# Kernel tuning notes

Hardware: AMD Instinct MI355X
Metric: run time of the kernel (lower is better)

The kernel has to match this reference:

```python
import jax, jax.numpy as jnp
import numpy as np

ROTARY_DIM = 64
ROPE_THETA = 10000.0
BLOCK_SIZE = 24


def setup_inputs() -> dict:
    key = jax.random.key(0)
    ks = jax.random.split(key, 6)
    B, T_code = 2, 2048
    d_cond, d_code, d_spk, d_model, vocab = 512, 512, 192, 1024, 6561
    cond = jax.random.normal(ks[0], (B, 1, d_cond), dtype=jnp.float32)
    spk = jax.random.normal(ks[1], (B, 1, d_spk), dtype=jnp.float32)
    code = jax.random.randint(ks[2], (B, T_code), 0, vocab, dtype=jnp.int64)
    embed_table = jax.random.normal(ks[3], (vocab, d_code), dtype=jnp.float32)
    W = jax.random.normal(ks[4], (d_cond + d_code + d_spk, d_model), dtype=jnp.float32) * 0.02
    b = jax.random.normal(ks[5], (d_model,), dtype=jnp.float32) * 0.02
    return {"cond": cond, "spk": spk, "code": code,
            "embed_table": embed_table, "W": W, "b": b}


def _rope(T):
    # DitRotary.forward
    pos = jnp.arange(T, dtype=jnp.float32).reshape(-1, 1)          # [T,1]
    theta = 1.0 / ROPE_THETA ** (jnp.arange(0, ROTARY_DIM, 2, dtype=jnp.float32) / ROTARY_DIM)
    idx = pos * theta                                              # [T,32]
    r = jnp.stack([jnp.cos(idx), jnp.sin(idx)])                    # [2,T,32]
    r = jnp.stack((r, r), axis=-1).reshape(2, T, ROTARY_DIM)       # [2,T,64]
    return r[:, None, :, None, :]                                  # [2,1,T,1,64]


def reference(cond, spk, code, embed_table, W, b):
    B, T_code = code.shape
    T = T_code * 2  # max_duration
    d_cond = cond.shape[-1]
    d_code = embed_table.shape[-1]
    code_embed = jnp.repeat(embed_table[code], 2, axis=1)          # [B,T,d_code]
    # concat([cond.repeat, code_embed, spk.repeat]) @ W + b, computed as split
    # matmuls with broadcast (same math, avoids materializing repeats)
    W_cond = W[:d_cond]
    W_code = W[d_cond:d_cond + d_code]
    W_spk = W[d_cond + d_code:]
    code_embeds = (jnp.einsum('btc,cd->btd', code_embed, W_code)
                   + cond @ W_cond + spk @ W_spk + b)              # [B,T,d_model]
    rope = _rope(T)
    # block-causal mask precompute
    blk = jnp.arange(T) // BLOCK_SIZE
    mask = (blk[None, :] - blk[:, None]).reshape(1, 1, T, T)       # int
    return code_embeds, rope, mask
```

## Files before the change

kernel.cpp:

```cpp
#include <hip/hip_runtime.h>
#include <hip/hip_bf16.h>
#include <cstdint>

typedef short short8 __attribute__((ext_vector_type(8)));
typedef float f32x4 __attribute__((ext_vector_type(4)));

#define OUT0_SZ  (2*4096*1024)
#define OUT1_OFF OUT0_SZ
#define OUT2_OFF (OUT0_SZ + 2*4096*64)

__device__ __forceinline__ unsigned short f2bf(float f) {
    unsigned u = __float_as_uint(f);
    unsigned r = (u + 0x7FFFu + ((u >> 16) & 1u)) >> 16;
    return (unsigned short)r;
}

__global__ __launch_bounds__(256) void prep_kernel(
    const float* __restrict__ embed, const int* __restrict__ code,
    const float* __restrict__ cond, const float* __restrict__ spk,
    const float* __restrict__ W, const float* __restrict__ bvec,
    unsigned short* __restrict__ Ag, unsigned short* __restrict__ Wt,
    float* __restrict__ bias)
{
    __shared__ float tile[32][33];
    __shared__ float red[8][32];
    const int bid = blockIdx.x;

    if (bid < 1024) {
        int gtid = bid * 256 + threadIdx.x;
        int r = gtid >> 6;
        int c = (gtid & 63) * 8;
        int cv = code[r];
        const float* s = embed + (size_t)cv * 512 + c;
        float4 f0 = *(const float4*)s;
        float4 f1 = *(const float4*)(s + 4);
        short8 v;
        v[0] = (short)f2bf(f0.x); v[1] = (short)f2bf(f0.y);
        v[2] = (short)f2bf(f0.z); v[3] = (short)f2bf(f0.w);
        v[4] = (short)f2bf(f1.x); v[5] = (short)f2bf(f1.y);
        v[6] = (short)f2bf(f1.z); v[7] = (short)f2bf(f1.w);
        *(short8*)&Ag[(size_t)r * 512 + c] = v;
    } else if (bid < 1536) {
        int idx = bid - 1024;
        int k0 = (idx & 15) * 32;
        int n0 = (idx >> 4) * 32;
        int lx = threadIdx.x & 31;
        int ly = threadIdx.x >> 5;
        #pragma unroll
        for (int rr = 0; rr < 32; rr += 8)
            tile[ly + rr][lx] = W[(size_t)(512 + k0 + ly + rr) * 1024 + n0 + lx];
        __syncthreads();
        #pragma unroll
        for (int rr = 0; rr < 32; rr += 8)
            Wt[(size_t)(n0 + ly + rr) * 512 + k0 + lx] = f2bf(tile[lx][ly + rr]);
    } else {
        int idx = bid - 1536;
        const int b  = idx >> 5;
        const int d0 = (idx & 31) * 32;
        const int dl = threadIdx.x & 31;
        const int ks = threadIdx.x >> 5;
        const int d  = d0 + dl;
        const float* condb = cond + b * 512;
        const float* spkb  = spk + b * 192;
        float acc = 0.f;
        #pragma unroll 8
        for (int i = 0; i < 64; ++i) {
            int k = ks * 64 + i;
            acc = fmaf(condb[k], W[(size_t)k * 1024 + d], acc);
        }
        #pragma unroll 8
        for (int i = 0; i < 24; ++i) {
            int s = ks * 24 + i;
            acc = fmaf(spkb[s], W[(size_t)(1024 + s) * 1024 + d], acc);
        }
        red[ks][dl] = acc;
        __syncthreads();
        if (ks == 0) {
            float t = acc + bvec[d];
            #pragma unroll
            for (int j = 1; j < 8; ++j) t += red[j][dl];
            bias[b * 1024 + d] = t;
        }
    }
}

__global__ __launch_bounds__(256) void main_kernel(
    const unsigned short* __restrict__ Ag, const unsigned short* __restrict__ Wt,
    const float* __restrict__ bias, float* __restrict__ out0,
    float* __restrict__ out1, float* __restrict__ out2)
{
    __shared__ short8 AsV[128 * 64 / 8];
    __shared__ short8 BsV[128 * 64 / 8];
    const int bid = blockIdx.x;

    if (bid < 256) {
        unsigned short* As = (unsigned short*)AsV;
        unsigned short* Bs = (unsigned short*)BsV;
        const int tid = threadIdx.x;
        const int bm = bid >> 3;
        const int bn = bid & 7;
        const int lane = tid & 63;
        const int wid = tid >> 6;
        const int wr = wid >> 1;
        const int wc = wid & 1;
        const int l15 = lane & 15;
        const int l4  = lane >> 4;

        f32x4 acc[4][4];
        #pragma unroll
        for (int i = 0; i < 4; ++i)
            #pragma unroll
            for (int j = 0; j < 4; ++j)
                acc[i][j] = (f32x4){0.f, 0.f, 0.f, 0.f};

        long a_off[4]; long b_off[4]; int dst[4];
        #pragma unroll
        for (int i = 0; i < 4; ++i) {
            int ch = i * 256 + tid;
            int r  = ch >> 3;
            int kc = (ch & 7) * 8;
            a_off[i] = (long)(bm * 128 + r) * 512 + kc;
            b_off[i] = (long)(bn * 128 + r) * 512 + kc;
            dst[i]   = r * 64 + (kc ^ ((r & 7) << 3));
        }

        for (int kt = 0; kt < 512; kt += 64) {
            __syncthreads();
            #pragma unroll
            for (int i = 0; i < 4; ++i)
                *(short8*)&As[dst[i]] = *(const short8*)&Ag[a_off[i] + kt];
            #pragma unroll
            for (int i = 0; i < 4; ++i)
                *(short8*)&Bs[dst[i]] = *(const short8*)&Wt[b_off[i] + kt];
            __syncthreads();
            #pragma unroll
            for (int ks = 0; ks < 2; ++ks) {
                const int kb = ks * 32 + l4 * 8;
                short8 af[4], bf[4];
                #pragma unroll
                for (int mi = 0; mi < 4; ++mi) {
                    int r = wr * 64 + mi * 16 + l15;
                    af[mi] = *(const short8*)&As[r * 64 + (kb ^ ((r & 7) << 3))];
                }
                #pragma unroll
                for (int ni = 0; ni < 4; ++ni) {
                    int n = wc * 64 + ni * 16 + l15;
                    bf[ni] = *(const short8*)&Bs[n * 64 + (kb ^ ((n & 7) << 3))];
                }
                #pragma unroll
                for (int mi = 0; mi < 4; ++mi)
                    #pragma unroll
                    for (int ni = 0; ni < 4; ++ni)
                        acc[mi][ni] = __builtin_amdgcn_mfma_f32_16x16x32_bf16(
                            af[mi], bf[ni], acc[mi][ni], 0, 0, 0);
            }
        }

        const int b = bm >> 4;
        const float* biasb = bias + b * 1024;
        #pragma unroll
        for (int ni = 0; ni < 4; ++ni) {
            const int n = bn * 128 + wc * 64 + ni * 16 + l15;
            const float bv = biasb[n];
            #pragma unroll
            for (int mi = 0; mi < 4; ++mi) {
                const int mbase = bm * 128 + wr * 64 + mi * 16 + l4 * 4;
                #pragma unroll
                for (int j = 0; j < 4; ++j) {
                    const int u = (mbase + j) & 2047;
                    const size_t o = ((size_t)(b * 4096 + 2 * u)) * 1024 + n;
                    const float v = acc[mi][ni][j] + bv;
                    out0[o] = v;
                    out0[o + 1024] = v;
                }
            }
        }
    } else if (bid < 1280) {
        int tid = (bid - 256) * 256 + threadIdx.x;
        int kk = tid & 31;
        int t  = (tid >> 5) & 4095;
        int c  = tid >> 17;
        double theta = exp2(-(double)kk * 0.41524101186092028);
        double a = (double)t * theta;
        float vf = (float)(c ? sin(a) : cos(a));
        float2 w; w.x = vf; w.y = vf;
        *(float2*)&out1[(size_t)(c * 4096 + t) * 64 + kk * 2] = w;
    } else {
        int q0 = (bid - 1280) * 1024 + threadIdx.x * 4;
        #pragma unroll
        for (int s = 0; s < 4; ++s) {
            int q = q0 + s;
            int i = q >> 10;
            int j = (q & 1023) << 2;
            int bi = i / 24;
            float4 v;
            v.x = (float)((j    ) / 24 - bi);
            v.y = (float)((j + 1) / 24 - bi);
            v.z = (float)((j + 2) / 24 - bi);
            v.w = (float)((j + 3) / 24 - bi);
            ((float4*)out2)[q] = v;
        }
    }
}

extern "C" void kernel_launch(void* const* d_in, const int* in_sizes, int n_in,
                              void* d_out, int out_size, void* d_ws, size_t ws_size,
                              hipStream_t stream) {
    const float* cond  = (const float*)d_in[0];
    const float* spk   = (const float*)d_in[1];
    const int*   code  = (const int*)d_in[2];
    const float* embed = (const float*)d_in[3];
    const float* W     = (const float*)d_in[4];
    const float* bvec  = (const float*)d_in[5];

    float* out  = (float*)d_out;
    float* out0 = out;
    float* out1 = out + OUT1_OFF;
    float* out2 = out + OUT2_OFF;

    float* bias = (float*)d_ws;
    unsigned short* Wt = (unsigned short*)((char*)d_ws + 8192);
    unsigned short* Ag = (unsigned short*)((char*)d_ws + 8192 + 1048576);

    prep_kernel<<<1600, 256, 0, stream>>>(embed, code, cond, spk, W, bvec,
                                          Ag, Wt, bias);
    main_kernel<<<5376, 256, 0, stream>>>(Ag, Wt, bias, out0, out1, out2);
}
```

Before: 155.4 us.

## Double-buffer GEMM tiles via direct global-to-LDS loads with pre-swizzled operands

The prep kernel now writes the bf16 activation and transposed weight matrices with the XOR swizzle already applied in global memory. The GEMM loop can then use global_load_lds to copy 16-byte chunks straight into shared memory without passing through registers. Shared memory is double-buffered so the next K-tile is fetched while MFMAs run on the current one, cutting one barrier per iteration. This doubles LDS use per block, which may lower occupancy, and it depends on the global-to-LDS builtin placing data in the expected layout.

```diff
diff --git a/kernel.cpp b/kernel.cpp
--- a/kernel.cpp
+++ b/kernel.cpp
@@ -14,6 +14,11 @@
     unsigned r = (u + 0x7FFFu + ((u >> 16) & 1u)) >> 16;
     return (unsigned short)r;
 }
+
+#define GLOAD_LDS(gp, lp)                                                     \
+    __builtin_amdgcn_global_load_lds(                                         \
+        (const __attribute__((address_space(1))) void*)(gp),                  \
+        (__attribute__((address_space(3))) void*)(lp), 16, 0, 0)
 
 __global__ __launch_bounds__(256) void prep_kernel(
     const float* __restrict__ embed, const int* __restrict__ code,
@@ -29,9 +34,9 @@
     if (bid < 1024) {
         int gtid = bid * 256 + threadIdx.x;
         int r = gtid >> 6;
-        int c = (gtid & 63) * 8;
+        int c = gtid & 63;
         int cv = code[r];
-        const float* s = embed + (size_t)cv * 512 + c;
+        const float* s = embed + (size_t)cv * 512 + c * 8;
         float4 f0 = *(const float4*)s;
         float4 f1 = *(const float4*)(s + 4);
         short8 v;
@@ -39,7 +44,8 @@
         v[2] = (short)f2bf(f0.z); v[3] = (short)f2bf(f0.w);
         v[4] = (short)f2bf(f1.x); v[5] = (short)f2bf(f1.y);
         v[6] = (short)f2bf(f1.z); v[7] = (short)f2bf(f1.w);
-        *(short8*)&Ag[(size_t)r * 512 + c] = v;
+        int csw = (c & ~7) | ((c & 7) ^ (r & 7));
+        *(short8*)&Ag[(size_t)r * 512 + csw * 8] = v;
     } else if (bid < 1536) {
         int idx = bid - 1024;
         int k0 = (idx & 15) * 32;
@@ -51,8 +57,12 @@
             tile[ly + rr][lx] = W[(size_t)(512 + k0 + ly + rr) * 1024 + n0 + lx];
         __syncthreads();
         #pragma unroll
-        for (int rr = 0; rr < 32; rr += 8)
-            Wt[(size_t)(n0 + ly + rr) * 512 + k0 + lx] = f2bf(tile[lx][ly + rr]);
+        for (int rr = 0; rr < 32; rr += 8) {
+            int n = n0 + ly + rr;
+            int k = k0 + lx;
+            int ksw = (k & ~63) | ((((k >> 3) & 7) ^ (n & 7)) << 3) | (k & 7);
+            Wt[(size_t)n * 512 + ksw] = f2bf(tile[lx][ly + rr]);
+        }
     } else {
         int idx = bid - 1536;
         const int b  = idx >> 5;
@@ -89,22 +99,25 @@
     const float* __restrict__ bias, float* __restrict__ out0,
     float* __restrict__ out1, float* __restrict__ out2)
 {
-    __shared__ short8 AsV[128 * 64 / 8];
-    __shared__ short8 BsV[128 * 64 / 8];
+    __shared__ unsigned short AsX[2][128 * 64];
+    __shared__ unsigned short BsX[2][128 * 64];
     const int bid = blockIdx.x;
 
     if (bid < 256) {
-        unsigned short* As = (unsigned short*)AsV;
-        unsigned short* Bs = (unsigned short*)BsV;
         const int tid = threadIdx.x;
         const int bm = bid >> 3;
         const int bn = bid & 7;
         const int lane = tid & 63;
-        const int wid = tid >> 6;
-        const int wr = wid >> 1;
-        const int wc = wid & 1;
+        const int w   = tid >> 6;
+        const int wr = w >> 1;
+        const int wc = w & 1;
         const int l15 = lane & 15;
         const int l4  = lane >> 4;
+        const int sub = lane >> 3;
+        const int chk = lane & 7;
+
+        const unsigned short* Asrc = Ag + (size_t)(bm * 128) * 512;
+        const unsigned short* Bsrc = Wt + (size_t)(bn * 128) * 512;
 
         f32x4 acc[4][4];
         #pragma unroll
@@ -113,26 +126,32 @@
             for (int j = 0; j < 4; ++j)
                 acc[i][j] = (f32x4){0.f, 0.f, 0.f, 0.f};
 
-        long a_off[4]; long b_off[4]; int dst[4];
+        size_t goff[4];
         #pragma unroll
         for (int i = 0; i < 4; ++i) {
-            int ch = i * 256 + tid;
-            int r  = ch >> 3;
-            int kc = (ch & 7) * 8;
-            a_off[i] = (long)(bm * 128 + r) * 512 + kc;
-            b_off[i] = (long)(bn * 128 + r) * 512 + kc;
-            dst[i]   = r * 64 + (kc ^ ((r & 7) << 3));
-        }
-
-        for (int kt = 0; kt < 512; kt += 64) {
-            __syncthreads();
-            #pragma unroll
-            for (int i = 0; i < 4; ++i)
-                *(short8*)&As[dst[i]] = *(const short8*)&Ag[a_off[i] + kt];
-            #pragma unroll
-            for (int i = 0; i < 4; ++i)
-                *(short8*)&Bs[dst[i]] = *(const short8*)&Wt[b_off[i] + kt];
-            __syncthreads();
+            int rg = (w * 4 + i) * 8 + sub;
+            goff[i] = (size_t)rg * 512 + chk * 8;
+        }
+
+        #pragma unroll
+        for (int i = 0; i < 4; ++i) {
+            GLOAD_LDS(Asrc + goff[i], &AsX[0][(w * 4 + i) * 512]);
+            GLOAD_LDS(Bsrc + goff[i], &BsX[0][(w * 4 + i) * 512]);
+        }
+        __syncthreads();
+
+        int cur = 0;
+        for (int t = 0; t < 8; ++t) {
+            if (t < 7) {
+                const int kt = (t + 1) * 64;
+                #pragma unroll
+                for (int i = 0; i < 4; ++i) {
+                    GLOAD_LDS(Asrc + goff[i] + kt, &AsX[cur ^ 1][(w * 4 + i) * 512]);
+                    GLOAD_LDS(Bsrc + goff[i] + kt, &BsX[cur ^ 1][(w * 4 + i) * 512]);
+                }
+            }
+            const unsigned short* As = AsX[cur];
+            const unsigned short* Bs = BsX[cur];
             #pragma unroll
             for (int ks = 0; ks < 2; ++ks) {
                 const int kb = ks * 32 + l4 * 8;
@@ -154,6 +173,8 @@
                         acc[mi][ni] = __builtin_amdgcn_mfma_f32_16x16x32_bf16(
                             af[mi], bf[ni], acc[mi][ni], 0, 0, 0);
             }
+            __syncthreads();
+            cur ^= 1;
         }
 
         const int b = bm >> 4;
@@ -183,8 +204,8 @@
         double theta = exp2(-(double)kk * 0.41524101186092028);
         double a = (double)t * theta;
         float vf = (float)(c ? sin(a) : cos(a));
-        float2 w; w.x = vf; w.y = vf;
-        *(float2*)&out1[(size_t)(c * 4096 + t) * 64 + kk * 2] = w;
+        float2 wv; wv.x = vf; wv.y = vf;
+        *(float2*)&out1[(size_t)(c * 4096 + t) * 64 + kk * 2] = wv;
     } else {
         int q0 = (bid - 1280) * 1024 + threadIdx.x * 4;
         #pragma unroll
```

Measured after the change: 153.0 us. Within noise of the previous version (-1.5%).
